# Kernel tuning notes

Measured on AMD Instinct MI355X. Metric: run time of the kernel, lower is better.

Reference implementation:

```python
import jax, jax.numpy as jnp
import numpy as np

B, S, NX, H = 8, 1024, 1024, 16
D = NX // H  # head_features = 64
SCALE = True


def setup_inputs() -> dict:
    key = jax.random.key(0)
    k1, k2, k3 = jax.random.split(key, 3)
    x = jax.random.normal(k1, (B, S, NX), dtype=jnp.float32)
    w_attn = jax.random.normal(k2, (NX, 3 * NX), dtype=jnp.float32) * 0.02
    b_attn = jnp.zeros((3 * NX,), dtype=jnp.float32)
    w_proj = jax.random.normal(k3, (NX, NX), dtype=jnp.float32) * 0.02
    b_proj = jnp.zeros((NX,), dtype=jnp.float32)
    return {"x": x, "w_attn": w_attn, "b_attn": b_attn, "w_proj": w_proj, "b_proj": b_proj}


def _split_heads(t):
    # (B, S, NX) -> (B, H, S, D)
    return t.reshape(B, S, H, D).transpose(0, 2, 1, 3)


def reference(x, w_attn, b_attn, w_proj, b_proj):
    # fused QKV projection (Conv1D): addmm over flattened tokens
    qkv = x @ w_attn + b_attn                      # (B, S, 3*NX)
    q, k, v = jnp.split(qkv, 3, axis=-1)
    q = _split_heads(q)                            # (B, H, S, D)
    k = _split_heads(k)
    v = _split_heads(v)

    w = jnp.einsum("bhqd,bhkd->bhqk", q, k)        # full S x S scores
    if SCALE:
        w = w / jnp.sqrt(jnp.asarray(D, w.dtype))
    # causal mask applied exactly as in the source: multiply + big-negative subtract
    b = jnp.tril(jnp.ones((S, S), dtype=w.dtype))[None, None]
    w = w * b - 1e10 * (1.0 - b)
    w = jax.nn.softmax(w, axis=-1)                 # attn_pdrop = 0 (eval)
    a = jnp.einsum("bhqk,bhkd->bhqd", w, v)        # (B, H, S, D)

    # merge heads: (B, H, S, D) -> (B, S, NX)
    a = a.transpose(0, 2, 1, 3).reshape(B, S, NX)
    a = a @ w_proj + b_proj                        # c_proj; resid_pdrop = 0 (eval)
    return a
```

## Files before the change

kernel.cpp:

```cpp
#include <hip/hip_runtime.h>
#include <hip/hip_bf16.h>

#define BB 8
#define SS 1024
#define NXX 1024
#define HH 16
#define DD 64
#define MM (BB * SS)

typedef __attribute__((ext_vector_type(8))) short short8;
typedef __attribute__((ext_vector_type(4))) short short4v;
typedef __attribute__((ext_vector_type(4))) float float4v;

static __device__ inline short bf16bits(float v) {
    __hip_bfloat16 t = __float2bfloat16(v);
    return *reinterpret_cast<short*>(&t);
}

__global__ __launch_bounds__(256) void prep_kernel(
    const float* __restrict__ x, __hip_bfloat16* __restrict__ xb,
    const float* __restrict__ w_attn, __hip_bfloat16* __restrict__ wT_attn,
    const float* __restrict__ w_proj, __hip_bfloat16* __restrict__ wT_proj)
{
    __shared__ __hip_bfloat16 tile[32][33];
    const int blk = blockIdx.x;
    const int tid = threadIdx.x;

    if (blk < 8192) {
        int i = blk * 1024 + tid * 4;
        float4 v = *(const float4*)(x + i);
        xb[i + 0] = __float2bfloat16(v.x);
        xb[i + 1] = __float2bfloat16(v.y);
        xb[i + 2] = __float2bfloat16(v.z);
        xb[i + 3] = __float2bfloat16(v.w);
        return;
    }
    const float* W;
    __hip_bfloat16* Wt;
    int K, N, idx;
    if (blk < 8192 + 3072) { idx = blk - 8192;  W = w_attn; Wt = wT_attn; K = NXX; N = 3 * NXX; }
    else                   { idx = blk - 11264; W = w_proj; Wt = wT_proj; K = NXX; N = NXX; }
    const int k0 = (idx % (K / 32)) * 32;
    const int n0 = (idx / (K / 32)) * 32;
    const int tx = tid % 32;
    const int ty = tid / 32;
#pragma unroll
    for (int p = 0; p < 4; ++p) {
        int k = ty + p * 8;
        tile[k][tx] = __float2bfloat16(W[(size_t)(k0 + k) * N + n0 + tx]);
    }
    __syncthreads();
#pragma unroll
    for (int p = 0; p < 4; ++p) {
        int nn = ty + p * 8;
        Wt[(size_t)(n0 + nn) * K + k0 + tx] = tile[tx][nn];
    }
}

#define WAIT_LGKM0_FENCED()                                                    \
    asm volatile("s_waitcnt lgkmcnt(0)" ::: "memory");                         \
    __builtin_amdgcn_sched_barrier(0);

#define STAGE_A(DST, kk)                                                       \
    {                                                                          \
        _Pragma("unroll") for (int j_ = 0; j_ < LA; ++j_) {                    \
            const __hip_bfloat16* s_ = aSrc + (size_t)(j_ * 128) * K + (kk);   \
            char* d_ = (char*)(DST) + j_ * 8192 + (wave << 10);                \
            __builtin_amdgcn_global_load_lds(                                  \
                (const __attribute__((address_space(1))) void*)s_,             \
                (__attribute__((address_space(3))) void*)d_, 16, 0, 0);        \
        }                                                                      \
    }

#define STAGE_B(DST, kk)                                                       \
    {                                                                          \
        _Pragma("unroll") for (int j_ = 0; j_ < LB; ++j_) {                    \
            const __hip_bfloat16* s_ = bSrc + (size_t)(j_ * 128) * K + (kk);   \
            char* d_ = (char*)(DST) + j_ * 8192 + (wave << 10);                \
            __builtin_amdgcn_global_load_lds(                                  \
                (const __attribute__((address_space(1))) void*)s_,             \
                (__attribute__((address_space(3))) void*)d_, 16, 0, 0);        \
        }                                                                      \
    }

template <int MODE, int BM, int BN>
__global__ __launch_bounds__(512, 2) void gemm3b(
    const __hip_bfloat16* __restrict__ A,
    const __hip_bfloat16* __restrict__ Bt,
    const float* __restrict__ bias,
    void* __restrict__ Cv,
    __hip_bfloat16* __restrict__ vT,
    int M, int K, int N)
{
    constexpr int NWM = BM / 64;
    constexpr int NWN = 8 / NWM;
    constexpr int WCOLS = BN / NWN;
    constexpr int NF = WCOLS / 16;
    constexpr int ASZ = BM * 64;
    constexpr int BSZ = BN * 64;
    constexpr int LA = BM / 128;
    constexpr int LB = BN / 128;

    extern __shared__ __attribute__((aligned(16))) char smem[];

    const int tid  = threadIdx.x;
    const int wave = tid >> 6;
    const int lane = tid & 63;
    const int wm = (wave / NWN) * 64;
    const int wn = (wave % NWN) * WCOLS;

    const int nwg = (int)gridDim.x;
    const int cpx = nwg >> 3;
    const int bid = (int)blockIdx.x;
    const int swz = (bid & 7) * cpx + (bid >> 3);
    const int ntN = N / BN;
    const int width = ntN << 3;
    const int group = swz / width;
    const int w = swz % width;
    const int m0 = (group * 8 + (w & 7)) * BM;
    const int n0 = (w >> 3) * BN;

    const int NT = K >> 5;

    const int row_s  = tid >> 2;
    const int srccol = (((tid & 3) ^ ((tid >> 3) & 3)) << 3);
    const __hip_bfloat16* aSrc = A  + (size_t)(m0 + row_s) * K + srccol;
    const __hip_bfloat16* bSrc = Bt + (size_t)(n0 + row_s) * K + srccol;

    const int l15 = lane & 15, q4 = lane >> 4;
    const int sslot = (q4 ^ ((l15 >> 1) & 3)) << 4;
    const int offA = (wm + l15) * 64 + sslot;
    const int offB = (wn + l15) * 64 + sslot;

    float4v acc[4][NF];
#pragma unroll
    for (int i = 0; i < 4; ++i)
#pragma unroll
        for (int j = 0; j < NF; ++j) acc[i][j] = (float4v){0.f, 0.f, 0.f, 0.f};

    char* const Abuf0 = (char*)smem;
    char* const Bbuf0 = (char*)smem + 3 * ASZ;

    STAGE_A(Abuf0,       0);
    STAGE_B(Bbuf0,       0);
    STAGE_A(Abuf0 + ASZ, 32);
    STAGE_B(Bbuf0 + BSZ, 32);
    asm volatile("s_waitcnt vmcnt(3)" ::: "memory");
    __builtin_amdgcn_s_barrier();

    int ia = 0;
    for (int t = 0; t < NT; ++t) {
        const char* Ab = Abuf0 + ia * ASZ;
        const char* Bb = Bbuf0 + ia * BSZ;
        const int ia2 = (ia >= 1) ? ia - 1 : 2;

        short8 a[4], b[NF];
#pragma unroll
        for (int mf = 0; mf < 4; ++mf) a[mf] = *(const short8*)(Ab + offA + mf * 1024);
#pragma unroll
        for (int nf = 0; nf < NF; ++nf) b[nf] = *(const short8*)(Bb + offB + nf * 1024);

        if (t + 2 < NT) {
            STAGE_A(Abuf0 + ia2 * ASZ, (t + 2) << 5);
            STAGE_B(Bbuf0 + ia2 * BSZ, (t + 2) << 5);
            asm volatile("s_waitcnt vmcnt(3)" ::: "memory");
        } else if (t + 1 < NT) {
            asm volatile("s_waitcnt vmcnt(0)" ::: "memory");
        }
        __builtin_amdgcn_s_barrier();
        WAIT_LGKM0_FENCED();
        __builtin_amdgcn_s_setprio(1);
#pragma unroll
        for (int mf = 0; mf < 4; ++mf)
#pragma unroll
            for (int nf = 0; nf < NF; ++nf)
                acc[mf][nf] = __builtin_amdgcn_mfma_f32_16x16x32_bf16(
                    a[mf], b[nf], acc[mf][nf], 0, 0, 0);
        __builtin_amdgcn_s_setprio(0);
        __builtin_amdgcn_s_barrier();

        ia = (ia == 2) ? 0 : ia + 1;
    }

    const int cr = q4 * 4;
    const int cc = l15;

    if (MODE == 1 && n0 >= 2048) {
        const int bb = m0 / SS;
#pragma unroll
        for (int mf = 0; mf < 4; ++mf) {
            int grow = m0 + wm + mf * 16 + cr;
            int ssr = grow & (SS - 1);
#pragma unroll
            for (int nf = 0; nf < NF; ++nf) {
                int gcol = n0 + wn + nf * 16 + cc;
                float bv = bias[gcol];
                int col = gcol - 2048;
                int hh = col >> 6, dd = col & 63;
                short4v pk;
#pragma unroll
                for (int r = 0; r < 4; ++r) pk[r] = bf16bits(acc[mf][nf][r] + bv);
                *(short4v*)(vT + (size_t)((bb * HH + hh) * 64 + dd) * SS + ssr) = pk;
            }
        }
    } else {
        const float qs = (MODE == 1 && n0 < 1024) ? 0.125f : 1.0f;
#pragma unroll
        for (int mf = 0; mf < 4; ++mf) {
            int grow = m0 + wm + mf * 16 + cr;
#pragma unroll
            for (int nf = 0; nf < NF; ++nf) {
                int gcol = n0 + wn + nf * 16 + cc;
                float bv = bias[gcol];
#pragma unroll
                for (int r = 0; r < 4; ++r) {
                    float v = (acc[mf][nf][r] + bv) * qs;
                    if constexpr (MODE == 1)
                        ((__hip_bfloat16*)Cv)[(size_t)(grow + r) * N + gcol] =
                            __float2bfloat16(v);
                    else
                        ((float*)Cv)[(size_t)(grow + r) * N + gcol] = v;
                }
            }
        }
    }
}

#define WAIT_VMCNT_LT()                                                        \
    if constexpr (LT == 3) { asm volatile("s_waitcnt vmcnt(3)" ::: "memory"); }\
    else                   { asm volatile("s_waitcnt vmcnt(2)" ::: "memory"); }

template <int MODE, int BM, int BN>
__global__ __launch_bounds__(512, 2) void gemm256(
    const __hip_bfloat16* __restrict__ A,
    const __hip_bfloat16* __restrict__ Bt,
    const float* __restrict__ bias,
    void* __restrict__ Cv,
    __hip_bfloat16* __restrict__ vT,
    int M, int K, int N)
{
    constexpr int NWM = BM / 64;
    constexpr int NWN = 8 / NWM;
    constexpr int WCOLS = BN / NWN;
    constexpr int NF = WCOLS / 16;
    constexpr int ASZ = BM * 64;
    constexpr int BSZ = BN * 64;
    constexpr int LA = BM / 128;
    constexpr int LB = BN / 128;
    constexpr int LT = LA + LB;

    __shared__ __attribute__((aligned(16))) char smem[3 * ASZ + 2 * BSZ];

    const int tid  = threadIdx.x;
    const int wave = tid >> 6;
    const int lane = tid & 63;
    const int wm = (wave / NWN) * 64;
    const int wn = (wave % NWN) * WCOLS;

    const int nwg = (int)gridDim.x;
    const int cpx = nwg >> 3;
    const int bid = (int)blockIdx.x;
    const int swz = (bid & 7) * cpx + (bid >> 3);
    const int ntN = N / BN;
    const int width = ntN << 3;
    const int group = swz / width;
    const int w = swz % width;
    const int m0 = (group * 8 + (w & 7)) * BM;
    const int n0 = (w >> 3) * BN;

    const int NT = K >> 5;

    const int row_s  = tid >> 2;
    const int srccol = (((tid & 3) ^ ((tid >> 3) & 3)) << 3);
    const __hip_bfloat16* aSrc = A  + (size_t)(m0 + row_s) * K + srccol;
    const __hip_bfloat16* bSrc = Bt + (size_t)(n0 + row_s) * K + srccol;

    const int l15 = lane & 15, q4 = lane >> 4;
    const int sslot = (q4 ^ ((l15 >> 1) & 3)) << 4;
    const int offA = (wm + l15) * 64 + sslot;
    const int offB = (wn + l15) * 64 + sslot;

    float4v acc[4][NF];
#pragma unroll
    for (int i = 0; i < 4; ++i)
#pragma unroll
        for (int j = 0; j < NF; ++j) acc[i][j] = (float4v){0.f, 0.f, 0.f, 0.f};

    char* const Abuf0 = (char*)smem;
    char* const Bbuf0 = (char*)smem + 3 * ASZ;

    STAGE_A(Abuf0,       0);
    STAGE_B(Bbuf0,       0);
    STAGE_A(Abuf0 + ASZ, 32);
    STAGE_B(Bbuf0 + BSZ, 32);
    WAIT_VMCNT_LT();
    __builtin_amdgcn_s_barrier();

    int ia = 0;
    for (int t = 0; t < NT; ++t) {
        const char* Ab = Abuf0 + ia * ASZ;
        char* Bb = Bbuf0 + (t & 1) * BSZ;
        const int ia2 = (ia == 0) ? 2 : ia - 1;

        short8 a[4], b[NF];

#pragma unroll
        for (int mf = 0; mf < 2; ++mf) a[mf] = *(const short8*)(Ab + offA + mf * 1024);
#pragma unroll
        for (int nf = 0; nf < NF; ++nf) b[nf] = *(const short8*)(Bb + offB + nf * 1024);
        if (t + 2 < NT) STAGE_A(Abuf0 + ia2 * ASZ, (t + 2) << 5);
        __builtin_amdgcn_s_barrier();
        WAIT_LGKM0_FENCED();
        __builtin_amdgcn_s_setprio(1);
#pragma unroll
        for (int mf = 0; mf < 2; ++mf)
#pragma unroll
            for (int nf = 0; nf < NF; ++nf)
                acc[mf][nf] = __builtin_amdgcn_mfma_f32_16x16x32_bf16(
                    a[mf], b[nf], acc[mf][nf], 0, 0, 0);
        __builtin_amdgcn_s_setprio(0);
        __builtin_amdgcn_s_barrier();

#pragma unroll
        for (int mf = 2; mf < 4; ++mf) a[mf] = *(const short8*)(Ab + offA + mf * 1024);
        if (t + 2 < NT) {
            STAGE_B(Bb, (t + 2) << 5);
            WAIT_VMCNT_LT();
        } else if (t + 1 < NT) {
            asm volatile("s_waitcnt vmcnt(0)" ::: "memory");
        }
        __builtin_amdgcn_s_barrier();
        WAIT_LGKM0_FENCED();
        __builtin_amdgcn_s_setprio(1);
#pragma unroll
        for (int mf = 2; mf < 4; ++mf)
#pragma unroll
            for (int nf = 0; nf < NF; ++nf)
                acc[mf][nf] = __builtin_amdgcn_mfma_f32_16x16x32_bf16(
                    a[mf], b[nf], acc[mf][nf], 0, 0, 0);
        __builtin_amdgcn_s_setprio(0);
        __builtin_amdgcn_s_barrier();

        ia = (ia == 2) ? 0 : ia + 1;
    }

    const int cr = q4 * 4;
    const int cc = l15;

    if (MODE == 1 && n0 >= 2048) {
        const int bb = m0 / SS;
#pragma unroll
        for (int mf = 0; mf < 4; ++mf) {
            int grow = m0 + wm + mf * 16 + cr;
            int ssr = grow & (SS - 1);
#pragma unroll
            for (int nf = 0; nf < NF; ++nf) {
                int gcol = n0 + wn + nf * 16 + cc;
                float bv = bias[gcol];
                int col = gcol - 2048;
                int hh = col >> 6, dd = col & 63;
                short4v pk;
#pragma unroll
                for (int r = 0; r < 4; ++r) pk[r] = bf16bits(acc[mf][nf][r] + bv);
                *(short4v*)(vT + (size_t)((bb * HH + hh) * 64 + dd) * SS + ssr) = pk;
            }
        }
    } else {
        const float qs = (MODE == 1 && n0 < 1024) ? 0.125f : 1.0f;
#pragma unroll
        for (int mf = 0; mf < 4; ++mf) {
            int grow = m0 + wm + mf * 16 + cr;
#pragma unroll
            for (int nf = 0; nf < NF; ++nf) {
                int gcol = n0 + wn + nf * 16 + cc;
                float bv = bias[gcol];
#pragma unroll
                for (int r = 0; r < 4; ++r) {
                    float v = (acc[mf][nf][r] + bv) * qs;
                    if constexpr (MODE == 1)
                        ((__hip_bfloat16*)Cv)[(size_t)(grow + r) * N + gcol] =
                            __float2bfloat16(v);
                    else
                        ((float*)Cv)[(size_t)(grow + r) * N + gcol] = v;
                }
            }
        }
    }
}

#define PSTR 72

__global__ __launch_bounds__(256) void attn_mfma_kernel(
    const __hip_bfloat16* __restrict__ qkv,
    const __hip_bfloat16* __restrict__ vT,
    __hip_bfloat16* __restrict__ aout)
{
    const int bh = blockIdx.x;
    const int b = bh / HH, h = bh % HH;
    const int q0 = ((int)gridDim.y - 1 - (int)blockIdx.y) * 128;

    __shared__ __hip_bfloat16 Ks[64 * PSTR];
    __shared__ __hip_bfloat16 Vs[64 * PSTR];
    __shared__ __hip_bfloat16 Ps[4][32 * PSTR];

    const int tid  = threadIdx.x;
    const int wave = tid >> 6;
    const int lane = tid & 63;
    const int quad = lane >> 4;
    const int l16  = lane & 15;

    short8 qf[2][2];
#pragma unroll
    for (int t = 0; t < 2; ++t) {
        const __hip_bfloat16* qp = qkv +
            (size_t)(b * SS + q0 + wave * 32 + t * 16 + l16) * 3072 + h * 64 + quad * 8;
        qf[t][0] = *(const short8*)qp;
        qf[t][1] = *(const short8*)(qp + 32);
    }

    float4v o_acc[2][4];
    float l_acc[2][4];
#pragma unroll
    for (int t = 0; t < 2; ++t)
#pragma unroll
        for (int nt = 0; nt < 4; ++nt) o_acc[t][nt] = (float4v){0.f, 0.f, 0.f, 0.f};
#pragma unroll
    for (int t = 0; t < 2; ++t)
#pragma unroll
        for (int r = 0; r < 4; ++r) l_acc[t][r] = 0.f;

    const int sk  = tid & 63;
    const int sdo = (tid >> 6) * 16;
    const int vd  = tid >> 2;
    const int vko = (tid & 3) * 16;
    const int qmin_w = q0 + wave * 32;
    const int nkt = q0 / 64 + 2;

    for (int kt = 0; kt < nkt; ++kt) {
        const int k0 = kt * 64;
        __syncthreads();
        {
            const __hip_bfloat16* kr =
                qkv + (size_t)(b * SS + k0 + sk) * 3072 + 1024 + h * 64 + sdo;
            *(short8*)&Ks[sk * PSTR + sdo]     = *(const short8*)kr;
            *(short8*)&Ks[sk * PSTR + sdo + 8] = *(const short8*)(kr + 8);
            const __hip_bfloat16* vr = vT + (size_t)(bh * 64 + vd) * SS + k0 + vko;
            *(short8*)&Vs[vd * PSTR + vko]     = *(const short8*)vr;
            *(short8*)&Vs[vd * PSTR + vko + 8] = *(const short8*)(vr + 8);
        }
        __syncthreads();
        if (k0 > qmin_w + 31) continue;

        const short* ks = (const short*)Ks;
        float4v sacc[2][4];
#pragma unroll
        for (int t = 0; t < 2; ++t)
#pragma unroll
            for (int nt = 0; nt < 4; ++nt) sacc[t][nt] = (float4v){0.f, 0.f, 0.f, 0.f};
#pragma unroll
        for (int kc = 0; kc < 2; ++kc)
#pragma unroll
            for (int nt = 0; nt < 4; ++nt) {
                short8 kb = *(const short8*)(ks + (nt * 16 + l16) * PSTR + kc * 32 + quad * 8);
                sacc[0][nt] = __builtin_amdgcn_mfma_f32_16x16x32_bf16(qf[0][kc], kb, sacc[0][nt], 0, 0, 0);
                sacc[1][nt] = __builtin_amdgcn_mfma_f32_16x16x32_bf16(qf[1][kc], kb, sacc[1][nt], 0, 0, 0);
            }

        const bool needmask = (k0 + 63 > qmin_w);
        __hip_bfloat16* pw = Ps[wave];
#pragma unroll
        for (int t = 0; t < 2; ++t)
#pragma unroll
            for (int nt = 0; nt < 4; ++nt) {
                int kk = k0 + nt * 16 + l16;
#pragma unroll
                for (int r = 0; r < 4; ++r) {
                    float s = sacc[t][nt][r];
                    if (needmask) {
                        int qq = qmin_w + t * 16 + quad * 4 + r;
                        if (kk > qq) s = -1e10f;
                    }
                    float p = __expf(s);
                    l_acc[t][r] += p;
                    pw[(t * 16 + quad * 4 + r) * PSTR + nt * 16 + l16] =
                        __float2bfloat16(p);
                }
            }

        const short* ps = (const short*)pw;
        const short* vs = (const short*)Vs;
#pragma unroll
        for (int kc = 0; kc < 2; ++kc) {
            short8 pa0 = *(const short8*)(ps + (0 * 16 + l16) * PSTR + kc * 32 + quad * 8);
            short8 pa1 = *(const short8*)(ps + (1 * 16 + l16) * PSTR + kc * 32 + quad * 8);
#pragma unroll
            for (int nt = 0; nt < 4; ++nt) {
                short8 vb = *(const short8*)(vs + (nt * 16 + l16) * PSTR + kc * 32 + quad * 8);
                o_acc[0][nt] = __builtin_amdgcn_mfma_f32_16x16x32_bf16(pa0, vb, o_acc[0][nt], 0, 0, 0);
                o_acc[1][nt] = __builtin_amdgcn_mfma_f32_16x16x32_bf16(pa1, vb, o_acc[1][nt], 0, 0, 0);
            }
        }
    }

#pragma unroll
    for (int t = 0; t < 2; ++t)
#pragma unroll
        for (int r = 0; r < 4; ++r) {
            float l = l_acc[t][r];
            l += __shfl_xor(l, 1);
            l += __shfl_xor(l, 2);
            l += __shfl_xor(l, 4);
            l += __shfl_xor(l, 8);
            float inv = 1.f / l;
            int row = q0 + wave * 32 + t * 16 + quad * 4 + r;
            __hip_bfloat16* op = aout + (size_t)(b * SS + row) * NXX + h * 64 + l16;
#pragma unroll
            for (int nt = 0; nt < 4; ++nt)
                op[nt * 16] = __float2bfloat16(o_acc[t][nt][r] * inv);
        }
}

extern "C" void kernel_launch(void* const* d_in, const int* in_sizes, int n_in,
                              void* d_out, int out_size, void* d_ws, size_t ws_size,
                              hipStream_t stream)
{
    const float* x      = (const float*)d_in[0];
    const float* w_attn = (const float*)d_in[1];
    const float* b_attn = (const float*)d_in[2];
    const float* w_proj = (const float*)d_in[3];
    const float* b_proj = (const float*)d_in[4];
    float* out = (float*)d_out;

    char* ws = (char*)d_ws;
    __hip_bfloat16* qkv     = (__hip_bfloat16*)ws;
    __hip_bfloat16* vT      = (__hip_bfloat16*)(ws + (size_t)48 * 1024 * 1024);
    __hip_bfloat16* xb      = (__hip_bfloat16*)(ws + (size_t)64 * 1024 * 1024);
    __hip_bfloat16* amid    = xb;
    __hip_bfloat16* wT_attn = (__hip_bfloat16*)(ws + (size_t)80 * 1024 * 1024);
    __hip_bfloat16* wT_proj = (__hip_bfloat16*)(ws + (size_t)86 * 1024 * 1024);

    constexpr int DYN_LDS = 3 * (256 * 64) + 3 * (128 * 64);
    static int dyn_state = 0;
    if (dyn_state == 0) {
        hipError_t e1 = hipFuncSetAttribute(
            reinterpret_cast<const void*>(&gemm3b<1, 256, 128>),
            hipFuncAttributeMaxDynamicSharedMemorySize, DYN_LDS);
        hipError_t e2 = hipFuncSetAttribute(
            reinterpret_cast<const void*>(&gemm3b<0, 256, 128>),
            hipFuncAttributeMaxDynamicSharedMemorySize, DYN_LDS);
        dyn_state = (e1 == hipSuccess && e2 == hipSuccess) ? 1 : -1;
        (void)hipGetLastError();
    }

    prep_kernel<<<dim3(12288), dim3(256), 0, stream>>>(
        x, xb, w_attn, wT_attn, w_proj, wT_proj);

    if (dyn_state == 1) {
        gemm3b<1, 256, 128><<<dim3((MM / 256) * ((3 * NXX) / 128)), dim3(512),
                              DYN_LDS, stream>>>(
            xb, wT_attn, b_attn, qkv, vT, MM, NXX, 3 * NXX);
    } else {
        gemm256<1, 256, 128><<<dim3((MM / 256) * ((3 * NXX) / 128)), dim3(512), 0, stream>>>(
            xb, wT_attn, b_attn, qkv, vT, MM, NXX, 3 * NXX);
    }

    attn_mfma_kernel<<<dim3(BB * HH, SS / 128), dim3(256), 0, stream>>>(qkv, vT, amid);

    if (dyn_state == 1) {
        gemm3b<0, 256, 128><<<dim3((MM / 256) * (NXX / 128)), dim3(512),
                              DYN_LDS, stream>>>(
            amid, wT_proj, b_proj, out, nullptr, MM, NXX, NXX);
    } else {
        gemm256<0, 256, 128><<<dim3((MM / 256) * (NXX / 128)), dim3(512), 0, stream>>>(
            amid, wT_proj, b_proj, out, nullptr, MM, NXX, NXX);
    }
}
```

Baseline: 216.2 us.

## Split-K the output projection GEMM into two slices plus a reduction kernel

Replaces the output projection GEMM (256 tiles) with a split-K version that runs 512 blocks, each covering half of K. The first slice writes partial sums plus bias to a workspace buffer and the second writes to the output. A separate add kernel then sums the two. The aim is better occupancy of the GPU's compute units, since 256 tiles underfill the device. In exchange it adds extra fp32 partial-sum traffic (write, read, rewrite of 32MB) and one more kernel launch.

```diff
diff --git a/kernel.cpp b/kernel.cpp
--- a/kernel.cpp
+++ b/kernel.cpp
@@ -223,6 +223,132 @@
                 }
             }
         }
+    }
+}
+
+__global__ __launch_bounds__(512, 2) void gemm_splitk(
+    const __hip_bfloat16* __restrict__ A,
+    const __hip_bfloat16* __restrict__ Bt,
+    const float* __restrict__ bias,
+    float* __restrict__ P0,
+    float* __restrict__ out)
+{
+    constexpr int BM = 256, BN = 128;
+    constexpr int NF = 4;
+    constexpr int ASZ = BM * 64;
+    constexpr int BSZ = BN * 64;
+    constexpr int LA = BM / 128;
+    constexpr int LB = BN / 128;
+    const int K = 1024;
+    const int NT = 16;
+
+    extern __shared__ __attribute__((aligned(16))) char smem[];
+
+    const int tid  = threadIdx.x;
+    const int wave = tid >> 6;
+    const int lane = tid & 63;
+    const int wm = (wave >> 1) * 64;
+    const int wn = (wave & 1) * 64;
+
+    const int slice = (int)blockIdx.x >> 8;
+    const int bid   = (int)blockIdx.x & 255;
+    const int koff  = slice << 9;
+
+    const int cpx = 32;
+    const int swz = (bid & 7) * cpx + (bid >> 3);
+    const int width = 64;
+    const int group = swz / width;
+    const int w = swz % width;
+    const int m0 = (group * 8 + (w & 7)) * BM;
+    const int n0 = (w >> 3) * BN;
+
+    const int row_s  = tid >> 2;
+    const int srccol = (((tid & 3) ^ ((tid >> 3) & 3)) << 3);
+    const __hip_bfloat16* aSrc = A  + (size_t)(m0 + row_s) * K + koff + srccol;
+    const __hip_bfloat16* bSrc = Bt + (size_t)(n0 + row_s) * K + koff + srccol;
+
+    const int l15 = lane & 15, q4 = lane >> 4;
+    const int sslot = (q4 ^ ((l15 >> 1) & 3)) << 4;
+    const int offA = (wm + l15) * 64 + sslot;
+    const int offB = (wn + l15) * 64 + sslot;
+
+    float4v acc[4][NF];
+#pragma unroll
+    for (int i = 0; i < 4; ++i)
+#pragma unroll
+        for (int j = 0; j < NF; ++j) acc[i][j] = (float4v){0.f, 0.f, 0.f, 0.f};
+
+    char* const Abuf0 = (char*)smem;
+    char* const Bbuf0 = (char*)smem + 3 * ASZ;
+
+    STAGE_A(Abuf0,       0);
+    STAGE_B(Bbuf0,       0);
+    STAGE_A(Abuf0 + ASZ, 32);
+    STAGE_B(Bbuf0 + BSZ, 32);
+    asm volatile("s_waitcnt vmcnt(3)" ::: "memory");
+    __builtin_amdgcn_s_barrier();
+
+    int ia = 0;
+    for (int t = 0; t < NT; ++t) {
+        const char* Ab = Abuf0 + ia * ASZ;
+        const char* Bb = Bbuf0 + ia * BSZ;
+        const int ia2 = (ia >= 1) ? ia - 1 : 2;
+
+        short8 a[4], b[NF];
+#pragma unroll
+        for (int mf = 0; mf < 4; ++mf) a[mf] = *(const short8*)(Ab + offA + mf * 1024);
+#pragma unroll
+        for (int nf = 0; nf < NF; ++nf) b[nf] = *(const short8*)(Bb + offB + nf * 1024);
+
+        if (t + 2 < NT) {
+            STAGE_A(Abuf0 + ia2 * ASZ, (t + 2) << 5);
+            STAGE_B(Bbuf0 + ia2 * BSZ, (t + 2) << 5);
+            asm volatile("s_waitcnt vmcnt(3)" ::: "memory");
+        } else if (t + 1 < NT) {
+            asm volatile("s_waitcnt vmcnt(0)" ::: "memory");
+        }
+        __builtin_amdgcn_s_barrier();
+        WAIT_LGKM0_FENCED();
+        __builtin_amdgcn_s_setprio(1);
+#pragma unroll
+        for (int mf = 0; mf < 4; ++mf)
+#pragma unroll
+            for (int nf = 0; nf < NF; ++nf)
+                acc[mf][nf] = __builtin_amdgcn_mfma_f32_16x16x32_bf16(
+                    a[mf], b[nf], acc[mf][nf], 0, 0, 0);
+        __builtin_amdgcn_s_setprio(0);
+        __builtin_amdgcn_s_barrier();
+
+        ia = (ia == 2) ? 0 : ia + 1;
+    }
+
+    const int cr = q4 * 4;
+    const int cc = l15;
+    float* dst = slice ? out : P0;
+#pragma unroll
+    for (int mf = 0; mf < 4; ++mf) {
+        int grow = m0 + wm + mf * 16 + cr;
+#pragma unroll
+        for (int nf = 0; nf < NF; ++nf) {
+            int gcol = n0 + wn + nf * 16 + cc;
+            float bv = slice ? 0.f : bias[gcol];
+#pragma unroll
+            for (int r = 0; r < 4; ++r)
+                dst[(size_t)(grow + r) * NXX + gcol] = acc[mf][nf][r] + bv;
+        }
+    }
+}
+
+__global__ __launch_bounds__(256) void addout(
+    float* __restrict__ out, const float* __restrict__ P0)
+{
+    size_t base = ((size_t)blockIdx.x * 256 + threadIdx.x) * 16;
+#pragma unroll
+    for (int j = 0; j < 4; ++j) {
+        float4 a = *(const float4*)(out + base + j * 4);
+        float4 b = *(const float4*)(P0 + base + j * 4);
+        a.x += b.x; a.y += b.y; a.z += b.z; a.w += b.w;
+        *(float4*)(out + base + j * 4) = a;
     }
 }
 
@@ -533,6 +659,7 @@
 
     char* ws = (char*)d_ws;
     __hip_bfloat16* qkv     = (__hip_bfloat16*)ws;
+    float*          P0      = (float*)ws;
     __hip_bfloat16* vT      = (__hip_bfloat16*)(ws + (size_t)48 * 1024 * 1024);
     __hip_bfloat16* xb      = (__hip_bfloat16*)(ws + (size_t)64 * 1024 * 1024);
     __hip_bfloat16* amid    = xb;
@@ -546,7 +673,7 @@
             reinterpret_cast<const void*>(&gemm3b<1, 256, 128>),
             hipFuncAttributeMaxDynamicSharedMemorySize, DYN_LDS);
         hipError_t e2 = hipFuncSetAttribute(
-            reinterpret_cast<const void*>(&gemm3b<0, 256, 128>),
+            reinterpret_cast<const void*>(&gemm_splitk),
             hipFuncAttributeMaxDynamicSharedMemorySize, DYN_LDS);
         dyn_state = (e1 == hipSuccess && e2 == hipSuccess) ? 1 : -1;
         (void)hipGetLastError();
@@ -567,9 +694,9 @@
     attn_mfma_kernel<<<dim3(BB * HH, SS / 128), dim3(256), 0, stream>>>(qkv, vT, amid);
 
     if (dyn_state == 1) {
-        gemm3b<0, 256, 128><<<dim3((MM / 256) * (NXX / 128)), dim3(512),
-                              DYN_LDS, stream>>>(
-            amid, wT_proj, b_proj, out, nullptr, MM, NXX, NXX);
+        gemm_splitk<<<dim3(512), dim3(512), DYN_LDS, stream>>>(
+            amid, wT_proj, b_proj, P0, out);
+        addout<<<dim3(2048), dim3(256), 0, stream>>>(out, P0);
     } else {
         gemm256<0, 256, 128><<<dim3((MM / 256) * (NXX / 128)), dim3(512), 0, stream>>>(
             amid, wT_proj, b_proj, out, nullptr, MM, NXX, NXX);
```

Result: slower. 239.6 us (+10.8%).

## Double-buffer attention K/V tiles via direct global-to-LDS loads with XOR swizzle

Applied to the files above, without the earlier changes.

The attention kernel now keeps two K/V shared-memory buffers. It prefetches the next 64-key tile with global_load_lds while MFMA work runs on the current tile. The padded row layout is replaced by an XOR-swizzled 64-wide layout so the 16-byte direct LDS writes avoid bank conflicts, and the two syncthreads per tile are replaced by a waitcnt plus a single barrier. This hides global load latency behind compute, at the cost of twice the K/V LDS footprint and manual synchronisation that must stay correct.

```diff
diff --git a/kernel.cpp b/kernel.cpp
--- a/kernel.cpp
+++ b/kernel.cpp
@@ -399,8 +399,8 @@
     const int b = bh / HH, h = bh % HH;
     const int q0 = ((int)gridDim.y - 1 - (int)blockIdx.y) * 128;
 
-    __shared__ __hip_bfloat16 Ks[64 * PSTR];
-    __shared__ __hip_bfloat16 Vs[64 * PSTR];
+    __shared__ __attribute__((aligned(16))) __hip_bfloat16 Ks[2][64 * 64];
+    __shared__ __attribute__((aligned(16))) __hip_bfloat16 Vs[2][64 * 64];
     __shared__ __hip_bfloat16 Ps[4][32 * PSTR];
 
     const int tid  = threadIdx.x;
@@ -429,77 +429,98 @@
 #pragma unroll
         for (int r = 0; r < 4; ++r) l_acc[t][r] = 0.f;
 
-    const int sk  = tid & 63;
-    const int sdo = (tid >> 6) * 16;
-    const int vd  = tid >> 2;
-    const int vko = (tid & 3) * 16;
+    const int srow = tid >> 3;
+    const int sslot8 = ((tid & 7) ^ (srow & 7)) * 8;
+
     const int qmin_w = q0 + wave * 32;
     const int nkt = q0 / 64 + 2;
 
+#define ASTAGE(KT, BUF)                                                        \
+    {                                                                          \
+        const int k0_ = (KT) * 64;                                             \
+        _Pragma("unroll") for (int j_ = 0; j_ < 2; ++j_) {                     \
+            const __hip_bfloat16* ks_ = qkv +                                  \
+                (size_t)(b * SS + k0_ + j_ * 32 + srow) * 3072 + 1024 +        \
+                h * 64 + sslot8;                                               \
+            __builtin_amdgcn_global_load_lds(                                  \
+                (const __attribute__((address_space(1))) void*)ks_,            \
+                (__attribute__((address_space(3))) void*)                      \
+                    ((char*)&Ks[BUF][0] + j_ * 4096 + tid * 16), 16, 0, 0);    \
+            const __hip_bfloat16* vs_ = vT +                                   \
+                (size_t)(bh * 64 + j_ * 32 + srow) * SS + k0_ + sslot8;        \
+            __builtin_amdgcn_global_load_lds(                                  \
+                (const __attribute__((address_space(1))) void*)vs_,            \
+                (__attribute__((address_space(3))) void*)                      \
+                    ((char*)&Vs[BUF][0] + j_ * 4096 + tid * 16), 16, 0, 0);    \
+        }                                                                      \
+    }
+
+    ASTAGE(0, 0);
+    asm volatile("s_waitcnt vmcnt(0)" ::: "memory");
+    __builtin_amdgcn_s_barrier();
+
+    int cur = 0;
     for (int kt = 0; kt < nkt; ++kt) {
         const int k0 = kt * 64;
-        __syncthreads();
-        {
-            const __hip_bfloat16* kr =
-                qkv + (size_t)(b * SS + k0 + sk) * 3072 + 1024 + h * 64 + sdo;
-            *(short8*)&Ks[sk * PSTR + sdo]     = *(const short8*)kr;
-            *(short8*)&Ks[sk * PSTR + sdo + 8] = *(const short8*)(kr + 8);
-            const __hip_bfloat16* vr = vT + (size_t)(bh * 64 + vd) * SS + k0 + vko;
-            *(short8*)&Vs[vd * PSTR + vko]     = *(const short8*)vr;
-            *(short8*)&Vs[vd * PSTR + vko + 8] = *(const short8*)(vr + 8);
-        }
-        __syncthreads();
-        if (k0 > qmin_w + 31) continue;
-
-        const short* ks = (const short*)Ks;
-        float4v sacc[2][4];
-#pragma unroll
-        for (int t = 0; t < 2; ++t)
-#pragma unroll
-            for (int nt = 0; nt < 4; ++nt) sacc[t][nt] = (float4v){0.f, 0.f, 0.f, 0.f};
-#pragma unroll
-        for (int kc = 0; kc < 2; ++kc)
-#pragma unroll
-            for (int nt = 0; nt < 4; ++nt) {
-                short8 kb = *(const short8*)(ks + (nt * 16 + l16) * PSTR + kc * 32 + quad * 8);
-                sacc[0][nt] = __builtin_amdgcn_mfma_f32_16x16x32_bf16(qf[0][kc], kb, sacc[0][nt], 0, 0, 0);
-                sacc[1][nt] = __builtin_amdgcn_mfma_f32_16x16x32_bf16(qf[1][kc], kb, sacc[1][nt], 0, 0, 0);
-            }
-
-        const bool needmask = (k0 + 63 > qmin_w);
-        __hip_bfloat16* pw = Ps[wave];
-#pragma unroll
-        for (int t = 0; t < 2; ++t)
-#pragma unroll
-            for (int nt = 0; nt < 4; ++nt) {
-                int kk = k0 + nt * 16 + l16;
-#pragma unroll
-                for (int r = 0; r < 4; ++r) {
-                    float s = sacc[t][nt][r];
-                    if (needmask) {
-                        int qq = qmin_w + t * 16 + quad * 4 + r;
-                        if (kk > qq) s = -1e10f;
+        if (kt + 1 < nkt) ASTAGE(kt + 1, cur ^ 1);
+
+        if (k0 <= qmin_w + 31) {
+            const char* ksb = (const char*)&Ks[cur][0];
+            float4v sacc[2][4];
+#pragma unroll
+            for (int t = 0; t < 2; ++t)
+#pragma unroll
+                for (int nt = 0; nt < 4; ++nt) sacc[t][nt] = (float4v){0.f, 0.f, 0.f, 0.f};
+#pragma unroll
+            for (int kc = 0; kc < 2; ++kc)
+#pragma unroll
+                for (int nt = 0; nt < 4; ++nt) {
+                    short8 kb = *(const short8*)(ksb + (nt * 16 + l16) * 128 +
+                        (((kc * 4 + quad) ^ (l16 & 7)) << 4));
+                    sacc[0][nt] = __builtin_amdgcn_mfma_f32_16x16x32_bf16(qf[0][kc], kb, sacc[0][nt], 0, 0, 0);
+                    sacc[1][nt] = __builtin_amdgcn_mfma_f32_16x16x32_bf16(qf[1][kc], kb, sacc[1][nt], 0, 0, 0);
+                }
+
+            const bool needmask = (k0 + 63 > qmin_w);
+            __hip_bfloat16* pw = Ps[wave];
+#pragma unroll
+            for (int t = 0; t < 2; ++t)
+#pragma unroll
+                for (int nt = 0; nt < 4; ++nt) {
+                    int kk = k0 + nt * 16 + l16;
+#pragma unroll
+                    for (int r = 0; r < 4; ++r) {
+                        float s = sacc[t][nt][r];
+                        if (needmask) {
+                            int qq = qmin_w + t * 16 + quad * 4 + r;
+                            if (kk > qq) s = -1e10f;
+                        }
+                        float p = __expf(s);
+                        l_acc[t][r] += p;
+                        pw[(t * 16 + quad * 4 + r) * PSTR + nt * 16 + l16] =
+                            __float2bfloat16(p);
                     }
-                    float p = __expf(s);
-                    l_acc[t][r] += p;
-                    pw[(t * 16 + quad * 4 + r) * PSTR + nt * 16 + l16] =
-                        __float2bfloat16(p);
+                }
+
+            const short* ps = (const short*)pw;
+            const char* vsb = (const char*)&Vs[cur][0];
+#pragma unroll
+            for (int kc = 0; kc < 2; ++kc) {
+                short8 pa0 = *(const short8*)(ps + (0 * 16 + l16) * PSTR + kc * 32 + quad * 8);
+                short8 pa1 = *(const short8*)(ps + (1 * 16 + l16) * PSTR + kc * 32 + quad * 8);
+#pragma unroll
+                for (int nt = 0; nt < 4; ++nt) {
+                    short8 vb = *(const short8*)(vsb + (nt * 16 + l16) * 128 +
+                        (((kc * 4 + quad) ^ (l16 & 7)) << 4));
+                    o_acc[0][nt] = __builtin_amdgcn_mfma_f32_16x16x32_bf16(pa0, vb, o_acc[0][nt], 0, 0, 0);
+                    o_acc[1][nt] = __builtin_amdgcn_mfma_f32_16x16x32_bf16(pa1, vb, o_acc[1][nt], 0, 0, 0);
                 }
             }
-
-        const short* ps = (const short*)pw;
-        const short* vs = (const short*)Vs;
-#pragma unroll
-        for (int kc = 0; kc < 2; ++kc) {
-            short8 pa0 = *(const short8*)(ps + (0 * 16 + l16) * PSTR + kc * 32 + quad * 8);
-            short8 pa1 = *(const short8*)(ps + (1 * 16 + l16) * PSTR + kc * 32 + quad * 8);
-#pragma unroll
-            for (int nt = 0; nt < 4; ++nt) {
-                short8 vb = *(const short8*)(vs + (nt * 16 + l16) * PSTR + kc * 32 + quad * 8);
-                o_acc[0][nt] = __builtin_amdgcn_mfma_f32_16x16x32_bf16(pa0, vb, o_acc[0][nt], 0, 0, 0);
-                o_acc[1][nt] = __builtin_amdgcn_mfma_f32_16x16x32_bf16(pa1, vb, o_acc[1][nt], 0, 0, 0);
-            }
-        }
+        }
+
+        if (kt + 1 < nkt) asm volatile("s_waitcnt vmcnt(0)" ::: "memory");
+        __builtin_amdgcn_s_barrier();
+        cur ^= 1;
     }
 
 #pragma unroll
@@ -518,6 +539,7 @@
             for (int nt = 0; nt < 4; ++nt)
                 op[nt * 16] = __float2bfloat16(o_acc[t][nt][r] * inv);
         }
+#undef ASTAGE
 }
 
 extern "C" void kernel_launch(void* const* d_in, const int* in_sizes, int n_in,
```

After: 218.8 us. About the same (+1.2%).
